# Optimization experiments

Measured on AMD Instinct MI355X. Metric: run time of the kernel, lower is better.

The kernel has to match this reference:

```python
import jax, jax.numpy as jnp
import numpy as np


def setup_inputs() -> dict:
    key = jax.random.key(0)
    x = jax.random.normal(key, (64, 2048, 256), dtype=jnp.float32)
    return {"x": x, "window": 32, "strides": 1}


def reference(x, window, strides):
    # x: [B, T, F]. Sliding-window population std over time axis, per feature.
    B, T, F = x.shape
    # Window start offsets (static, from shapes) -- mirrors the keras loop:
    starts = list(range(0, T - window + 1, strides))
    if (T - window) not in starts:
        starts.append(T - window)
    idx = jnp.asarray(starts, dtype=jnp.int32)  # [S]

    # Prefix sums of x and x^2 along time, with a leading zero row so that
    # windowed sum = c[start+window] - c[start].  One pass instead of
    # recomputing each overlapping window.
    zero = jnp.zeros((B, 1, F), dtype=x.dtype)
    c1 = jnp.concatenate([zero, jnp.cumsum(x, axis=1)], axis=1)          # [B, T+1, F]
    c2 = jnp.concatenate([zero, jnp.cumsum(x * x, axis=1)], axis=1)      # [B, T+1, F]

    s1 = c1[:, idx + window, :] - c1[:, idx, :]  # [B, S, F] window sums
    s2 = c2[:, idx + window, :] - c2[:, idx, :]  # [B, S, F] window sums of squares

    inv_w = jnp.asarray(1.0 / window, dtype=x.dtype)
    mean = s1 * inv_w
    var = s2 * inv_w - mean * mean               # population variance (K.std is biased)
    std = jnp.sqrt(jnp.maximum(var, 0.0))
    # Original: K.switch(is_nan(std), mean - mean, std) -> NaN stds become 0.
    std = jnp.where(jnp.isnan(std), jnp.zeros_like(std), std)
    return std  # [B, S, F]
```

## Files before the change

### kernel.cpp

```cpp
#include <hip/hip_runtime.h>

#define B_DIM 64
#define T_DIM 2048
#define F_DIM 256
#define W_DIM 32
#define S_DIM (T_DIM - W_DIM + 1)
#define CHUNK 128
#define RUN   (CHUNK / 4)
#define F4    (F_DIM / 4)

__global__ __launch_bounds__(256) void ts_std_kernel(const float* __restrict__ x,
                                                     float* __restrict__ out) {
    const int tid = threadIdx.x;
    const int f4  = tid & (F4 - 1);
    const int sub = tid >> 6;
    const int b   = blockIdx.y;
    const int s0  = blockIdx.x * CHUNK + sub * RUN;
    if (s0 >= S_DIM) return;

    const float4* __restrict__ xp =
        (const float4*)(x + (size_t)b * T_DIM * F_DIM) + f4;
    float4* __restrict__ op =
        (float4*)(out + (size_t)b * S_DIM * F_DIM) + f4;

    float4 a1 = make_float4(0.f, 0.f, 0.f, 0.f);
    float4 a2 = make_float4(0.f, 0.f, 0.f, 0.f);
    #pragma unroll
    for (int w = 0; w < W_DIM; ++w) {
        float4 v = xp[(size_t)(s0 + w) * F4];
        a1.x += v.x; a1.y += v.y; a1.z += v.z; a1.w += v.w;
        a2.x += v.x * v.x; a2.y += v.y * v.y;
        a2.z += v.z * v.z; a2.w += v.w * v.w;
    }

    const float invw = 1.0f / (float)W_DIM;

    auto emit = [&](int s) {
        float4 r;
        {
            float m = a1.x * invw;
            r.x = sqrtf(fmaxf(fmaf(-m, m, a2.x * invw), 0.f));
        }
        {
            float m = a1.y * invw;
            r.y = sqrtf(fmaxf(fmaf(-m, m, a2.y * invw), 0.f));
        }
        {
            float m = a1.z * invw;
            r.z = sqrtf(fmaxf(fmaf(-m, m, a2.z * invw), 0.f));
        }
        {
            float m = a1.w * invw;
            r.w = sqrtf(fmaxf(fmaf(-m, m, a2.w * invw), 0.f));
        }
        op[(size_t)s * F4] = r;
    };

    emit(s0);

    const int nrun = (S_DIM - s0 < RUN) ? (S_DIM - s0) : RUN;
    #pragma unroll 4
    for (int r = 1; r < nrun; ++r) {
        float4 vn = xp[(size_t)(s0 + r + W_DIM - 1) * F4];
        float4 vo = xp[(size_t)(s0 + r - 1) * F4];
        a1.x += vn.x - vo.x; a1.y += vn.y - vo.y;
        a1.z += vn.z - vo.z; a1.w += vn.w - vo.w;
        a2.x += vn.x * vn.x - vo.x * vo.x;
        a2.y += vn.y * vn.y - vo.y * vo.y;
        a2.z += vn.z * vn.z - vo.z * vo.z;
        a2.w += vn.w * vn.w - vo.w * vo.w;
        emit(s0 + r);
    }
}

extern "C" void kernel_launch(void* const* d_in, const int* in_sizes, int n_in,
                              void* d_out, int out_size, void* d_ws, size_t ws_size,
                              hipStream_t stream) {
    const float* x = (const float*)d_in[0];
    float* out = (float*)d_out;

    dim3 grid((S_DIM + CHUNK - 1) / CHUNK, B_DIM);
    ts_std_kernel<<<grid, 256, 0, stream>>>(x, out);
}
```

Before: 252.1 us.

## Halve chunk size, use vector types and nontemporal output stores

Reduces CHUNK from 128 to 64, so each thread runs 16 sliding steps instead of 32 and the grid has twice as many blocks. Rewrites the arithmetic with ext_vector_type float4 and stores outputs with nontemporal hints so the large write stream bypasses cache retention. Loop unroll changes from 4 to 5. The shorter runs mean the 32-row window warmup is amortised over fewer outputs, raising redundant input reads; this is traded for more parallelism and cheaper stores.

```diff
diff --git a/kernel.cpp b/kernel.cpp
--- a/kernel.cpp
+++ b/kernel.cpp
@@ -5,9 +5,11 @@
 #define F_DIM 256
 #define W_DIM 32
 #define S_DIM (T_DIM - W_DIM + 1)
-#define CHUNK 128
+#define CHUNK 64
 #define RUN   (CHUNK / 4)
 #define F4    (F_DIM / 4)
+
+typedef float vfloat4 __attribute__((ext_vector_type(4)));
 
 __global__ __launch_bounds__(256) void ts_std_kernel(const float* __restrict__ x,
                                                      float* __restrict__ out) {
@@ -18,57 +20,42 @@
     const int s0  = blockIdx.x * CHUNK + sub * RUN;
     if (s0 >= S_DIM) return;
 
-    const float4* __restrict__ xp =
-        (const float4*)(x + (size_t)b * T_DIM * F_DIM) + f4;
-    float4* __restrict__ op =
-        (float4*)(out + (size_t)b * S_DIM * F_DIM) + f4;
+    const vfloat4* __restrict__ xp =
+        (const vfloat4*)(x + (size_t)b * T_DIM * F_DIM) + f4;
+    vfloat4* __restrict__ op =
+        (vfloat4*)(out + (size_t)b * S_DIM * F_DIM) + f4;
 
-    float4 a1 = make_float4(0.f, 0.f, 0.f, 0.f);
-    float4 a2 = make_float4(0.f, 0.f, 0.f, 0.f);
+    vfloat4 a1 = (vfloat4)0.f;
+    vfloat4 a2 = (vfloat4)0.f;
     #pragma unroll
     for (int w = 0; w < W_DIM; ++w) {
-        float4 v = xp[(size_t)(s0 + w) * F4];
-        a1.x += v.x; a1.y += v.y; a1.z += v.z; a1.w += v.w;
-        a2.x += v.x * v.x; a2.y += v.y * v.y;
-        a2.z += v.z * v.z; a2.w += v.w * v.w;
+        vfloat4 v = xp[(size_t)(s0 + w) * F4];
+        a1 += v;
+        a2 += v * v;
     }
 
     const float invw = 1.0f / (float)W_DIM;
 
     auto emit = [&](int s) {
-        float4 r;
-        {
-            float m = a1.x * invw;
-            r.x = sqrtf(fmaxf(fmaf(-m, m, a2.x * invw), 0.f));
-        }
-        {
-            float m = a1.y * invw;
-            r.y = sqrtf(fmaxf(fmaf(-m, m, a2.y * invw), 0.f));
-        }
-        {
-            float m = a1.z * invw;
-            r.z = sqrtf(fmaxf(fmaf(-m, m, a2.z * invw), 0.f));
-        }
-        {
-            float m = a1.w * invw;
-            r.w = sqrtf(fmaxf(fmaf(-m, m, a2.w * invw), 0.f));
-        }
-        op[(size_t)s * F4] = r;
+        vfloat4 m = a1 * invw;
+        vfloat4 v = a2 * invw - m * m;
+        vfloat4 r;
+        r.x = sqrtf(fmaxf(v.x, 0.f));
+        r.y = sqrtf(fmaxf(v.y, 0.f));
+        r.z = sqrtf(fmaxf(v.z, 0.f));
+        r.w = sqrtf(fmaxf(v.w, 0.f));
+        __builtin_nontemporal_store(r, &op[(size_t)s * F4]);
     };
 
     emit(s0);
 
     const int nrun = (S_DIM - s0 < RUN) ? (S_DIM - s0) : RUN;
-    #pragma unroll 4
+    #pragma unroll 5
     for (int r = 1; r < nrun; ++r) {
-        float4 vn = xp[(size_t)(s0 + r + W_DIM - 1) * F4];
-        float4 vo = xp[(size_t)(s0 + r - 1) * F4];
-        a1.x += vn.x - vo.x; a1.y += vn.y - vo.y;
-        a1.z += vn.z - vo.z; a1.w += vn.w - vo.w;
-        a2.x += vn.x * vn.x - vo.x * vo.x;
-        a2.y += vn.y * vn.y - vo.y * vo.y;
-        a2.z += vn.z * vn.z - vo.z * vo.z;
-        a2.w += vn.w * vn.w - vo.w * vo.w;
+        vfloat4 vn = xp[(size_t)(s0 + r + W_DIM - 1) * F4];
+        vfloat4 vo = xp[(size_t)(s0 + r - 1) * F4];
+        a1 += vn - vo;
+        a2 += vn * vn - vo * vo;
         emit(s0 + r);
     }
 }
```

Result: no change. 253.2 us (+0.4%).
